# Kernel optimization log

Measured on AMD Instinct MI355X. Metric: run time of the kernel, lower is better.

Reference implementation:

```python
import jax, jax.numpy as jnp
import numpy as np

# ProbSparseAttention (Informer-style), mask_flag=False, factor=10, scale=None,
# output_attention=False, dropout never applied in forward.
# L = 2048 -> U_part = u = 10 * ceil(log(2048)) = 80.
U_TOP = 80


def setup_inputs() -> dict:
    key = jax.random.key(0)
    kq, kk, kv, ki = jax.random.split(key, 4)
    B, L, H, D = 2, 2048, 8, 64
    sample_k = U_TOP
    queries = jax.random.normal(kq, (B, L, H, D), dtype=jnp.float32)
    keys = jax.random.normal(kk, (B, L, H, D), dtype=jnp.float32)
    values = jax.random.normal(kv, (B, L, H, D), dtype=jnp.float32)
    # replaces torch.randint(low=0, high=min(L_Q, L_K), size=(L_Q, sample_k))
    index_sample = jax.random.randint(ki, (L, sample_k), 0, L, dtype=jnp.int32)
    return {"queries": queries, "keys": keys, "values": values,
            "index_sample": index_sample}


def reference(queries, keys, values, index_sample):
    B, L_Q, H, D = queries.shape
    L_K = keys.shape[1]
    u = U_TOP  # n_top queries kept (== sample_k here)

    # [B, L, H, D] -> [B, H, L, D]
    Q = jnp.transpose(queries, (0, 2, 1, 3))
    K = jnp.transpose(keys, (0, 2, 1, 3))
    V = jnpp_transpose = jnp.transpose(values, (0, 2, 1, 3))

    # --- _prob_QK: gather sampled keys per query position ---
    # K_sample[b,h,l,s,:] = K[b,h,index_sample[l,s],:]  -> [B,H,L_Q,sample_k,D]
    K_sample = K[:, :, index_sample, :]
    # Q_K_sample: [B,H,L_Q,sample_k]
    Q_K_sample = jnp.einsum('bhld,bhlsd->bhls', Q, K_sample)
    # sparsity measure M = max - mean(sum/L_K)
    M = Q_K_sample.max(axis=-1) - Q_K_sample.sum(axis=-1) / L_K  # [B,H,L_Q]
    _, M_top = jax.lax.top_k(M, u)  # [B,H,u] indices of top queries

    # Q_reduce: [B,H,u,D]
    Q_reduce = jnp.take_along_axis(Q, M_top[..., None], axis=2)
    # sparse scores against ALL keys: [B,H,u,L_K]
    scale = 1.0 / np.sqrt(D).astype(np.float32)
    scores = jnp.einsum('bhud,bhkd->bhuk', Q_reduce, K) * scale

    # --- initial context (mask_flag=False): mean of V broadcast over u slots ---
    V_mean = V.mean(axis=2)  # [B,H,D]
    context = jnp.broadcast_to(V_mean[:, :, None, :], (B, H, u, D))

    # --- update context at selected slots ---
    attn = jax.nn.softmax(scores, axis=-1)          # [B,H,u,L_K]
    upd = jnp.einsum('bhuk,bhkd->bhud', attn, V)    # [B,H,u,D]
    # original clamps index into [0, L_slot-1] where L_slot = u
    idx = jnp.clip(M_top, 0, u - 1)
    b_idx = jnp.arange(B)[:, None, None]
    h_idx = jnp.arange(H)[None, :, None]
    context = context.at[b_idx, h_idx, idx, :].set(upd)

    # [B,H,u,D] -> [B,u,H,D]
    return jnp.transpose(context, (0, 2, 1, 3))
```

## Files before the change

### kernel.cpp

```cpp
#include <hip/hip_runtime.h>
#include <math.h>

#define LQ 2048
#define NH 8
#define DD 64
#define SK 80
#define UTOP 80
#define NB 2
#define CH 32
#define CK2 64
#define CKS 32

__global__ __launch_bounds__(256) void kA_M(const float* __restrict__ Q,
                                            const float* __restrict__ K,
                                            const int* __restrict__ idxs,
                                            float* __restrict__ M) {
    int b    = blockIdx.x & 1;
    int rid  = ((blockIdx.x >> 1) << 2) + (threadIdx.x >> 6);
    int lane = threadIdx.x & 63;
    int h = rid >> 11;
    int l = rid & 2047;
    int g = lane >> 4;
    int t = lane & 15;
    const float4* Qrow = (const float4*)(Q + (((size_t)(b * LQ + l) * NH + h) << 6));
    float4 q4 = Qrow[t];
    float maxv = -INFINITY, sumv = 0.f;
    const int* idxrow = idxs + l * SK;
#pragma unroll
    for (int it = 0; it < SK / 4; ++it) {
        int s = (it << 2) + g;
        int kidx = idxrow[s];
        const float4* Krow = (const float4*)(K + (((size_t)(b * LQ + kidx) * NH + h) << 6));
        float4 k4 = Krow[t];
        float p = q4.x * k4.x + q4.y * k4.y + q4.z * k4.z + q4.w * k4.w;
        p += __shfl_xor(p, 1, 16);
        p += __shfl_xor(p, 2, 16);
        p += __shfl_xor(p, 4, 16);
        p += __shfl_xor(p, 8, 16);
        maxv = fmaxf(maxv, p);
        sumv += p;
    }
    maxv = fmaxf(maxv, __shfl_xor(maxv, 16));
    maxv = fmaxf(maxv, __shfl_xor(maxv, 32));
    sumv += __shfl_xor(sumv, 16);
    sumv += __shfl_xor(sumv, 32);
    if (lane == 0) M[(b * NH + h) * LQ + l] = maxv - sumv * (1.f / 2048.f);
}

__global__ __launch_bounds__(256) void kB_topk(const float* __restrict__ M,
                                               int* __restrict__ Mtop,
                                               int* __restrict__ Winfo) {
    int bh = blockIdx.x;
    int tid = threadIdx.x;
    int lane = tid & 63, w = tid >> 6;
    __shared__ unsigned long long keys[LQ];
    __shared__ int hist[256];
    __shared__ int wavered[4];
    __shared__ int s_need;
    __shared__ unsigned long long s_prefix;
    __shared__ int s_cnt;
    __shared__ unsigned long long s_win;
    const float* Mrow = M + bh * LQ;
#pragma unroll
    for (int i = 0; i < 8; ++i) {
        int e = i * 256 + tid;
        unsigned int bits = __float_as_uint(Mrow[e]);
        bits ^= (unsigned int)(((int)bits >> 31)) | 0x80000000u;
        keys[e] = ((unsigned long long)bits << 16) | (unsigned int)(2047 - e);
    }
    if (tid == 0) { s_need = UTOP; s_prefix = 0ull; s_cnt = 0; s_win = ~0ull; }
    __syncthreads();
#pragma unroll
    for (int pass = 0; pass < 6; ++pass) {
        int shift = 40 - pass * 8;
        int need = s_need;
        unsigned long long pref = s_prefix;
        hist[tid] = 0;
        __syncthreads();
        unsigned long long prefmask = ~((1ull << (shift + 8)) - 1ull);
#pragma unroll
        for (int i = 0; i < 8; ++i) {
            unsigned long long k = keys[i * 256 + tid];
            if ((k & prefmask) == pref)
                atomicAdd(&hist[(int)((k >> shift) & 255)], 1);
        }
        __syncthreads();
        int b = 255 - tid;
        int v = hist[b];
        int x = v;
#pragma unroll
        for (int off = 1; off < 64; off <<= 1) {
            int y = __shfl_up(x, off);
            if (lane >= off) x += y;
        }
        if (lane == 63) wavered[w] = x;
        __syncthreads();
        int add = 0;
        for (int ww = 0; ww < w; ++ww) add += wavered[ww];
        int C = x + add;
        if (C >= need && C - v < need) {
            s_need = need - (C - v);
            s_prefix = pref | ((unsigned long long)b << shift);
        }
        __syncthreads();
    }
    unsigned long long kth = s_prefix;
#pragma unroll
    for (int i = 0; i < 8; ++i) {
        unsigned long long k = keys[i * 256 + tid];
        if (k >= kth) {
            int slot = atomicAdd(&s_cnt, 1);
            int q = 2047 - (int)(k & 0xffffu);
            Mtop[bh * UTOP + slot] = q;
            if (q >= UTOP - 1) atomicMin(&s_win, k);
        }
    }
    __syncthreads();
    if (tid == 0) Winfo[bh] = 2047 - (int)(s_win & 0xffffu);
}

__global__ __launch_bounds__(256) void kC_vsum(const float* __restrict__ V,
                                               float* __restrict__ Vsum) {
    int bh = blockIdx.x & 15;
    int b = bh & 1, h = bh >> 1;
    int lc = blockIdx.x >> 4;
    int d = threadIdx.x & 63;
    int lsub = threadIdx.x >> 6;
    float s = 0.f;
#pragma unroll 4
    for (int i = 0; i < 32; ++i) {
        int l = lc * 128 + lsub + (i << 2);
        s += V[(((size_t)(b * LQ + l) * NH + h) << 6) + d];
    }
    __shared__ float sc[256];
    sc[threadIdx.x] = s;
    __syncthreads();
    if (threadIdx.x < 64) {
        float tot = sc[threadIdx.x] + sc[threadIdx.x + 64] + sc[threadIdx.x + 128] + sc[threadIdx.x + 192];
        atomicAdd(&Vsum[(b * NH + h) * DD + d], tot);
    }
}

__global__ __launch_bounds__(256) void kD_attn(const float* __restrict__ Q,
                                               const float* __restrict__ K,
                                               const float* __restrict__ V,
                                               const int* __restrict__ Mtop,
                                               float* __restrict__ part_m,
                                               float* __restrict__ part_l,
                                               float* __restrict__ part_acc) {
    int code = blockIdx.x & 15;
    int b = code & 1, h = code >> 1;
    int bhl = b * NH + h;
    int c = blockIdx.x >> 4;
    __shared__ int topl[UTOP];
    __shared__ __align__(16) float Qs[UTOP][68];
    __shared__ __align__(16) float Ks[CKS][68];
    __shared__ __align__(16) float Vs[CKS][68];
    __shared__ float Ps[UTOP][33];
    int tid = threadIdx.x;
    if (tid < UTOP) topl[tid] = Mtop[bhl * UTOP + tid];
    __syncthreads();
    for (int f = tid; f < UTOP * 16; f += 256) {
        int u = f >> 4, t4 = f & 15;
        const float4* src = (const float4*)(Q + (((size_t)(b * LQ + topl[u]) * NH + h) << 6));
        *((float4*)&Qs[u][t4 << 2]) = src[t4];
    }
    int i = tid >> 4, j = tid & 15;
    const float scale = 0.125f;
    float4 acc[5];
    float m_run[5], l_run[5];
#pragma unroll
    for (int n = 0; n < 5; ++n) {
        acc[n] = make_float4(0.f, 0.f, 0.f, 0.f);
        m_run[n] = -INFINITY;
        l_run[n] = 0.f;
    }
    for (int sc = 0; sc < 2; ++sc) {
        __syncthreads();
        int kbase = c * CK2 + sc * CKS;
        for (int f = tid; f < CKS * 16; f += 256) {
            int k = f >> 4, t4 = f & 15;
            const float4* srck = (const float4*)(K + (((size_t)(b * LQ + kbase + k) * NH + h) << 6));
            *((float4*)&Ks[k][t4 << 2]) = srck[t4];
            const float4* srcv = (const float4*)(V + (((size_t)(b * LQ + kbase + k) * NH + h) << 6));
            *((float4*)&Vs[k][t4 << 2]) = srcv[t4];
        }
        __syncthreads();
        float s0[5], s1[5];
#pragma unroll
        for (int n = 0; n < 5; ++n) { s0[n] = 0.f; s1[n] = 0.f; }
#pragma unroll
        for (int d4 = 0; d4 < 16; ++d4) {
            float4 ka = *((float4*)&Ks[j][d4 << 2]);
            float4 kb = *((float4*)&Ks[j + 16][d4 << 2]);
#pragma unroll
            for (int n = 0; n < 5; ++n) {
                float4 q4 = *((float4*)&Qs[i * 5 + n][d4 << 2]);
                s0[n] += q4.x * ka.x + q4.y * ka.y + q4.z * ka.z + q4.w * ka.w;
                s1[n] += q4.x * kb.x + q4.y * kb.y + q4.z * kb.z + q4.w * kb.w;
            }
        }
        float m32[5], l32[5];
#pragma unroll
        for (int n = 0; n < 5; ++n) {
            float a = s0[n] * scale, bb = s1[n] * scale;
            float m = fmaxf(a, bb);
#pragma unroll
            for (int off = 1; off < 16; off <<= 1) m = fmaxf(m, __shfl_xor(m, off, 16));
            float p0 = __expf(a - m), p1 = __expf(bb - m);
            float ls = p0 + p1;
#pragma unroll
            for (int off = 1; off < 16; off <<= 1) ls += __shfl_xor(ls, off, 16);
            int u = i * 5 + n;
            Ps[u][j] = p0;
            Ps[u][j + 16] = p1;
            m32[n] = m;
            l32[n] = ls;
        }
        __syncthreads();
#pragma unroll
        for (int n = 0; n < 5; ++n) {
            float4 pv = make_float4(0.f, 0.f, 0.f, 0.f);
            int u = i * 5 + n;
            for (int k = 0; k < CKS; ++k) {
                float4 v4 = *((float4*)&Vs[k][j << 2]);
                float p = Ps[u][k];
                pv.x += p * v4.x; pv.y += p * v4.y; pv.z += p * v4.z; pv.w += p * v4.w;
            }
            float m_new = fmaxf(m_run[n], m32[n]);
            float fo = __expf(m_run[n] - m_new);
            float fn = __expf(m32[n] - m_new);
            l_run[n] = l_run[n] * fo + l32[n] * fn;
            acc[n].x = acc[n].x * fo + fn * pv.x;
            acc[n].y = acc[n].y * fo + fn * pv.y;
            acc[n].z = acc[n].z * fo + fn * pv.z;
            acc[n].w = acc[n].w * fo + fn * pv.w;
            m_run[n] = m_new;
        }
    }
#pragma unroll
    for (int n = 0; n < 5; ++n) {
        int u = i * 5 + n;
        size_t base = ((size_t)(bhl * CH + c) * UTOP + u);
        if (j == 0) {
            part_m[base] = m_run[n];
            part_l[base] = l_run[n];
        }
        *((float4*)&part_acc[base * DD + (j << 2)]) = acc[n];
    }
}

__global__ __launch_bounds__(64) void kE_combine(const float* __restrict__ part_m,
                                                 const float* __restrict__ part_l,
                                                 const float* __restrict__ part_acc,
                                                 float* __restrict__ upd) {
    int bhl = blockIdx.x & 15;
    int u = blockIdx.x >> 4;
    int lane = threadIdx.x;
    float mc = -INFINITY, lc = 0.f;
    if (lane < CH) {
        mc = part_m[(size_t)(bhl * CH + lane) * UTOP + u];
        lc = part_l[(size_t)(bhl * CH + lane) * UTOP + u];
    }
    float m = mc;
#pragma unroll
    for (int off = 1; off < 64; off <<= 1) m = fmaxf(m, __shfl_xor(m, off));
    float alpha = __expf(mc - m);
    float lsum = lc * alpha;
#pragma unroll
    for (int off = 1; off < 64; off <<= 1) lsum += __shfl_xor(lsum, off);
    float accd = 0.f;
    for (int c = 0; c < CH; ++c) {
        float a = __shfl(alpha, c);
        accd += a * part_acc[((size_t)(bhl * CH + c) * UTOP + u) * DD + lane];
    }
    upd[(size_t)(bhl * UTOP + u) * DD + lane] = accd / lsum;
}

__global__ __launch_bounds__(256) void kF_write(const int* __restrict__ Mtop,
                                                const int* __restrict__ Winfo,
                                                const float* __restrict__ upd,
                                                const float* __restrict__ Vsum,
                                                float* __restrict__ out) {
    int bhl = blockIdx.x;
    int b = bhl >> 3, h = bhl & 7;
    __shared__ int winner_row[UTOP];
    int tid = threadIdx.x;
    if (tid < UTOP) winner_row[tid] = -1;
    __syncthreads();
    if (tid < UTOP) {
        int q = Mtop[bhl * UTOP + tid];
        if (q < UTOP - 1) winner_row[q] = tid;
        if (q == Winfo[bhl]) winner_row[UTOP - 1] = tid;
    }
    __syncthreads();
    for (int f = tid; f < UTOP * DD; f += 256) {
        int r = f >> 6, d = f & 63;
        int w = winner_row[r];
        float val = (w >= 0) ? upd[(size_t)(bhl * UTOP + w) * DD + d]
                             : Vsum[bhl * DD + d] * (1.f / 2048.f);
        out[(((size_t)(b * UTOP + r)) * NH + h) * DD + d] = val;
    }
}

extern "C" void kernel_launch(void* const* d_in, const int* in_sizes, int n_in,
                              void* d_out, int out_size, void* d_ws, size_t ws_size,
                              hipStream_t stream) {
    const float* Q = (const float*)d_in[0];
    const float* K = (const float*)d_in[1];
    const float* V = (const float*)d_in[2];
    const int* idxs = (const int*)d_in[3];
    float* out = (float*)d_out;

    char* base = (char*)d_ws;
    float* M        = (float*)(base + 0);
    int*   Mtop     = (int*)  (base + 131072);
    int*   Winfo    = (int*)  (base + 136192);
    float* Vsum     = (float*)(base + 136256);
    float* part_m   = (float*)(base + 140352);
    float* part_l   = (float*)(base + 304192);
    float* part_acc = (float*)(base + 468032);
    float* upd      = (float*)(base + 10953792);

    hipMemsetAsync(Vsum, 0, NB * NH * DD * sizeof(float), stream);

    kA_M   <<<8192, 256, 0, stream>>>(Q, K, idxs, M);
    kB_topk<<<16,   256, 0, stream>>>(M, Mtop, Winfo);
    kC_vsum<<<256,  256, 0, stream>>>(V, Vsum);
    kD_attn<<<16 * CH, 256, 0, stream>>>(Q, K, V, Mtop, part_m, part_l, part_acc);
    kE_combine<<<16 * UTOP, 64, 0, stream>>>(part_m, part_l, part_acc, upd);
    kF_write<<<16, 256, 0, stream>>>(Mtop, Winfo, upd, Vsum, out);
}
```

Baseline: 146.6 us.

## Reorder kA block mapping by head and register-tile the P·V loop

The M-computation kernel now maps consecutive blocks across heads and batch before query position, which changes the order in which gathered K rows are touched, aiming for better cache locality. In the attention kernel, the P·V product is restructured so each V row loaded from shared memory is reused across all five query rows held by a thread. The P values are loaded as float4 from a padded 36-wide shared buffer. This cuts shared-memory loads per FMA but raises register pressure, and the new padding may change bank conflicts on the P stores.

```diff
diff --git a/kernel.cpp b/kernel.cpp
--- a/kernel.cpp
+++ b/kernel.cpp
@@ -15,11 +15,11 @@
                                             const float* __restrict__ K,
                                             const int* __restrict__ idxs,
                                             float* __restrict__ M) {
-    int b    = blockIdx.x & 1;
-    int rid  = ((blockIdx.x >> 1) << 2) + (threadIdx.x >> 6);
+    int x = blockIdx.x;
+    int h = x & 7;
+    int b = (x >> 3) & 1;
+    int l = ((x >> 4) << 2) + (threadIdx.x >> 6);
     int lane = threadIdx.x & 63;
-    int h = rid >> 11;
-    int l = rid & 2047;
     int g = lane >> 4;
     int t = lane & 15;
     const float4* Qrow = (const float4*)(Q + (((size_t)(b * LQ + l) * NH + h) << 6));
@@ -156,7 +156,7 @@
     __shared__ __align__(16) float Qs[UTOP][68];
     __shared__ __align__(16) float Ks[CKS][68];
     __shared__ __align__(16) float Vs[CKS][68];
-    __shared__ float Ps[UTOP][33];
+    __shared__ __align__(16) float Ps[UTOP][36];
     int tid = threadIdx.x;
     if (tid < UTOP) topl[tid] = Mtop[bhl * UTOP + tid];
     __syncthreads();
@@ -218,23 +218,38 @@
             l32[n] = ls;
         }
         __syncthreads();
+        float4 pv[5];
+#pragma unroll
+        for (int n = 0; n < 5; ++n) pv[n] = make_float4(0.f, 0.f, 0.f, 0.f);
+#pragma unroll
+        for (int kt = 0; kt < 4; ++kt) {
+            float4 pA[5], pB[5];
+#pragma unroll
+            for (int n = 0; n < 5; ++n) {
+                pA[n] = *((float4*)&Ps[i * 5 + n][kt * 8]);
+                pB[n] = *((float4*)&Ps[i * 5 + n][kt * 8 + 4]);
+            }
+#pragma unroll
+            for (int kk = 0; kk < 8; ++kk) {
+                float4 v4 = *((float4*)&Vs[kt * 8 + kk][j << 2]);
+#pragma unroll
+                for (int n = 0; n < 5; ++n) {
+                    float p = (kk < 4) ? ((float*)&pA[n])[kk] : ((float*)&pB[n])[kk - 4];
+                    pv[n].x += p * v4.x; pv[n].y += p * v4.y;
+                    pv[n].z += p * v4.z; pv[n].w += p * v4.w;
+                }
+            }
+        }
 #pragma unroll
         for (int n = 0; n < 5; ++n) {
-            float4 pv = make_float4(0.f, 0.f, 0.f, 0.f);
-            int u = i * 5 + n;
-            for (int k = 0; k < CKS; ++k) {
-                float4 v4 = *((float4*)&Vs[k][j << 2]);
-                float p = Ps[u][k];
-                pv.x += p * v4.x; pv.y += p * v4.y; pv.z += p * v4.z; pv.w += p * v4.w;
-            }
             float m_new = fmaxf(m_run[n], m32[n]);
             float fo = __expf(m_run[n] - m_new);
             float fn = __expf(m32[n] - m_new);
             l_run[n] = l_run[n] * fo + l32[n] * fn;
-            acc[n].x = acc[n].x * fo + fn * pv.x;
-            acc[n].y = acc[n].y * fo + fn * pv.y;
-            acc[n].z = acc[n].z * fo + fn * pv.z;
-            acc[n].w = acc[n].w * fo + fn * pv.w;
+            acc[n].x = acc[n].x * fo + fn * pv[n].x;
+            acc[n].y = acc[n].y * fo + fn * pv[n].y;
+            acc[n].z = acc[n].z * fo + fn * pv[n].z;
+            acc[n].w = acc[n].w * fo + fn * pv[n].w;
             m_run[n] = m_new;
         }
     }
```

New measurement: 146.6 us. Within noise of the previous version (-0.0%).
